# Optimization experiments

Measured on AMD Instinct MI355X. Metric: run time of the kernel, lower is better.

Reference implementation:

```python
import jax, jax.numpy as jnp
import numpy as np

N, E, F, B, L, C = 10000, 80000, 1024, 32, 800, 16
D = 128  # output_dim


def _lrelu(v):
    return jax.nn.leaky_relu(v, 0.01)


def _gcn(x, ei, W, b):
    # PyG GCNConv: add self-loops, symmetric norm D^-1/2 (A+I) D^-1/2, x@W then scatter, +bias
    loops = jnp.arange(N)
    row = jnp.concatenate([ei[0], loops])
    col = jnp.concatenate([ei[1], loops])
    deg = jax.ops.segment_sum(jnp.ones_like(row, x.dtype), col, num_segments=N)
    dinv = jnp.where(deg > 0, 1.0 / jnp.sqrt(jnp.maximum(deg, 1e-12)), 0.0)
    norm = dinv[row] * dinv[col]
    xw = x @ W  # [N,F]
    return jax.ops.segment_sum(xw[row] * norm[:, None], col, num_segments=N) + b


def _mean_pool(h, batch):
    s = jax.ops.segment_sum(h, batch, num_segments=B)
    c = jax.ops.segment_sum(jnp.ones((h.shape[0],), h.dtype), batch, num_segments=B)
    return s / jnp.maximum(c, 1.0)[:, None]


def _masif(ms, mf, sw, sb, fw, fb, Wfc, bfc):
    # mean over channels -> Conv1d(1,1,1) == scalar scale+shift -> relu
    s = jax.nn.relu(ms.mean(1) * sw[0] + sb[0])  # [B,L]
    f = jax.nn.relu(mf.mean(1) * fw[0] + fb[0])  # [B,L]
    m = jnp.stack([s, f], 1)                      # [B,2,L]
    m = m.reshape(B, 2, 80, L // 80).mean(-1)     # AdaptiveAvgPool1d(80), L % 80 == 0
    return m.mean(1) @ Wfc + bfc                  # [B,64]


def setup_inputs():
    key = jax.random.key(0)
    ks = jax.random.split(key, 48)
    def rn(i, shape, s=0.02):
        return jax.random.normal(ks[i], shape, jnp.float32) * s
    inp = {}
    inp['pro1_x'] = jax.random.normal(ks[0], (N, F), jnp.float32)
    inp['pro1_edge_index'] = jax.random.randint(ks[1], (2, E), 0, N)
    inp['pro1_batch'] = jnp.sort(jax.random.randint(ks[2], (N,), 0, B))
    inp['pro2_x'] = jax.random.normal(ks[3], (N, F), jnp.float32)
    inp['pro2_edge_index'] = jax.random.randint(ks[4], (2, E), 0, N)
    inp['pro2_batch'] = jnp.sort(jax.random.randint(ks[5], (N,), 0, B))
    for j, name in enumerate(['mas1_straight', 'mas1_flipped', 'mas2_straight', 'mas2_flipped']):
        inp[name] = jax.random.normal(ks[6 + j], (B, C, L), jnp.float32)
    inp['W_g1'] = rn(10, (F, F)); inp['b_g1'] = rn(11, (F,))
    inp['W_g2'] = rn(12, (F, F)); inp['b_g2'] = rn(13, (F,))
    inp['W_pf1'] = rn(14, (F, D)); inp['b_pf1'] = rn(15, (D,))
    inp['W_pf2'] = rn(16, (F, D)); inp['b_pf2'] = rn(17, (D,))
    inp['W_fc1'] = rn(18, (2 * D, 256)); inp['b_fc1'] = rn(19, (256,))
    inp['W_fc2'] = rn(20, (256, 64)); inp['b_fc2'] = rn(21, (64,))
    inp['cs1_w'] = rn(22, (1,), 1.0); inp['cs1_b'] = rn(23, (1,), 0.1)
    inp['cf1_w'] = rn(24, (1,), 1.0); inp['cf1_b'] = rn(25, (1,), 0.1)
    inp['cs2_w'] = rn(26, (1,), 1.0); inp['cs2_b'] = rn(27, (1,), 0.1)
    inp['cf2_w'] = rn(28, (1,), 1.0); inp['cf2_b'] = rn(29, (1,), 0.1)
    inp['W_m1'] = rn(30, (80, 64)); inp['b_m1'] = rn(31, (64,))
    inp['W_m2'] = rn(32, (80, 64)); inp['b_m2'] = rn(33, (64,))
    inp['W_out'] = rn(34, (192, 1)); inp['b_out'] = rn(35, (1,))
    return inp


def reference(pro1_x, pro1_edge_index, pro1_batch, pro2_x, pro2_edge_index, pro2_batch,
              mas1_straight, mas1_flipped, mas2_straight, mas2_flipped,
              W_g1, b_g1, W_g2, b_g2, W_pf1, b_pf1, W_pf2, b_pf2,
              W_fc1, b_fc1, W_fc2, b_fc2,
              cs1_w, cs1_b, cf1_w, cf1_b, cs2_w, cs2_b, cf2_w, cf2_b,
              W_m1, b_m1, W_m2, b_m2, W_out, b_out):
    # protein branch 1
    h1 = _lrelu(_gcn(pro1_x, pro1_edge_index, W_g1, b_g1))
    x1 = _lrelu(_mean_pool(h1, pro1_batch) @ W_pf1 + b_pf1)  # dropout = eval identity
    # protein branch 2
    h2 = _lrelu(_gcn(pro2_x, pro2_edge_index, W_g2, b_g2))
    x2 = _lrelu(_mean_pool(h2, pro2_batch) @ W_pf2 + b_pf2)
    xc = jnp.concatenate([x1, x2], 1)
    xc = _lrelu(xc @ W_fc1 + b_fc1)
    xc = _lrelu(xc @ W_fc2 + b_fc2)
    m1 = _masif(mas1_straight, mas1_flipped, cs1_w, cs1_b, cf1_w, cf1_b, W_m1, b_m1)
    m2 = _masif(mas2_straight, mas2_flipped, cs2_w, cs2_b, cf2_w, cf2_b, W_m2, b_m2)
    z = jnp.concatenate([xc, m1, m2], 1)  # [B,192]
    return jax.nn.sigmoid(z @ W_out + b_out)
```

## Files before the change

### kernel.cpp

```cpp
#include <hip/hip_runtime.h>
#include <hip/hip_bf16.h>
#include <math.h>

#define NNODES 10000
#define NEDGES 80000
#define FDIM   1024
#define BGR    32
#define LLEN   800
#define CCH    16
#define DDIM   128
#define NPAD2  10240
#define NE_BLK 625

typedef __attribute__((ext_vector_type(4))) _Float16 f16x4;
typedef __attribute__((ext_vector_type(8))) _Float16 f16x8;
typedef __attribute__((ext_vector_type(4))) float f32x4;
typedef __attribute__((ext_vector_type(2))) float f32x2;
typedef __attribute__((ext_vector_type(2))) long long2v;

__device__ __forceinline__ float lrelu(float v){ return v > 0.0f ? v : 0.01f*v; }

__global__ __launch_bounds__(256) void k_deg(const int* __restrict__ ei0, const int* __restrict__ ei1,
                                             int* __restrict__ cnt){
  int i = blockIdx.x*256 + threadIdx.x;
  int br = i >= NEDGES;
  int e  = br ? i - NEDGES : i;
  const int* ei = br ? ei1 : ei0;
  atomicAdd(&cnt[br*NNODES + ei[NEDGES + e]], 1);
}

__global__ __launch_bounds__(1024) void k_scan(const int* __restrict__ cnt, int* __restrict__ rowstart,
                                               float* __restrict__ dinv,
                                               const int* __restrict__ batch0,
                                               const int* __restrict__ batch1,
                                               int* __restrict__ bstart_){
  __shared__ int part[1024];
  const int br = blockIdx.x;
  const int* c = cnt + br*NNODES;
  int* rs = rowstart + br*(NNODES+1);
  float* dv = dinv + br*NNODES;
  const int* batch = br ? batch1 : batch0;
  int* bstart = bstart_ + br*(BGR+1);
  const int t = threadIdx.x;
  const int base = t*10;
  int local[10];
  int s = 0;
  #pragma unroll
  for (int i = 0; i < 10; ++i){
    int v = (base+i < NNODES) ? c[base+i] : 0;
    local[i] = s; s += v;
    if (base+i < NNODES) dv[base+i] = rsqrtf((float)v + 1.0f);
  }
  part[t] = s;
  __syncthreads();
  for (int off = 1; off < 1024; off <<= 1){
    int v = (t >= off) ? part[t-off] : 0;
    __syncthreads();
    part[t] += v;
    __syncthreads();
  }
  const int prev = (t == 0) ? 0 : part[t-1];
  #pragma unroll
  for (int i = 0; i < 10; ++i)
    if (base+i < NNODES) rs[base+i] = prev + local[i];
  if (t == 0) rs[NNODES] = NEDGES;
  for (int i = base; i < base+10 && i < NNODES; ++i){
    int b = batch[i];
    if (i == 0){ for (int bb = 0; bb <= b; ++bb) bstart[bb] = 0; }
    else {
      int pb = batch[i-1];
      if (b != pb) for (int bb = pb+1; bb <= b; ++bb) bstart[bb] = i;
    }
    if (i == NNODES-1){ for (int bb = b+1; bb <= BGR; ++bb) bstart[bb] = NNODES; }
  }
}

__global__ __launch_bounds__(256) void k_misc(const int* __restrict__ ei0, const int* __restrict__ ei1,
                                              const int* __restrict__ rowstart,
                                              int* __restrict__ cursor, int* __restrict__ csr,
                                              const float* __restrict__ x0, const float* __restrict__ x1,
                                              const float* __restrict__ dinv,
                                              unsigned char* __restrict__ xs8,
                                              const float* __restrict__ W0, const float* __restrict__ W1,
                                              unsigned char* __restrict__ Wt8,
                                              const float* __restrict__ ms1, const float* __restrict__ mf1,
                                              const float* __restrict__ ms2, const float* __restrict__ mf2,
                                              const float* __restrict__ sw1, const float* __restrict__ sb1,
                                              const float* __restrict__ fw1, const float* __restrict__ fb1,
                                              const float* __restrict__ sw2, const float* __restrict__ sb2,
                                              const float* __restrict__ fw2, const float* __restrict__ fb2,
                                              const float* __restrict__ Wm1, const float* __restrict__ bm1,
                                              const float* __restrict__ Wm2, const float* __restrict__ bm2,
                                              float* __restrict__ m12){
  __shared__ float tl[32][33];
  __shared__ float sf[LLEN];
  __shared__ float w80[80];
  const int bx = blockIdx.x, t = threadIdx.x;
  if (bx < NE_BLK){
    const int i = bx*256 + t;
    const int br = i >= NEDGES;
    const int e  = br ? i - NEDGES : i;
    const int* ei = br ? ei1 : ei0;
    const int r = ei[e], c = ei[NEDGES + e];
    const int pos = atomicAdd(&cursor[br*NNODES + c], 1);
    csr[br*NEDGES + rowstart[br*(NNODES+1) + c] + pos] = r;
  } else if (bx < NE_BLK + 2*NNODES){
    const int idx = bx - NE_BLK;
    const int br = idx >= NNODES;
    const int row = br ? idx - NNODES : idx;
    const float* x = (br ? x1 : x0) + (size_t)row*FDIM;
    unsigned char* o = xs8 + ((size_t)br*NNODES + row)*FDIM;
    const int f = t*4;
    const float d = dinv[br*NNODES + row];
    const float4 v = *(const float4*)(x + f);
    int p = __builtin_amdgcn_cvt_pk_fp8_f32(v.x*d, v.y*d, 0, false);
    p = __builtin_amdgcn_cvt_pk_fp8_f32(v.z*d, v.w*d, p, true);
    *(int*)(o + f) = p;
  } else if (bx < NE_BLK + 2*NNODES + 2048){
    const int idx = bx - NE_BLK - 2*NNODES;
    const int br = idx >> 10, tile = idx & 1023;
    const float* W = br ? W1 : W0;
    unsigned char* Wo = Wt8 + (size_t)br*FDIM*FDIM;
    const int k0 = (tile >> 5)*32, n0 = (tile & 31)*32;
    const int r = t >> 3, c4 = (t & 7)*4;
    const float4 v = *(const float4*)(W + (size_t)(k0+r)*FDIM + n0 + c4);
    tl[r][c4] = v.x; tl[r][c4+1] = v.y; tl[r][c4+2] = v.z; tl[r][c4+3] = v.w;
    __syncthreads();
    int p = __builtin_amdgcn_cvt_pk_fp8_f32(tl[c4  ][r], tl[c4+1][r], 0, false);
    p = __builtin_amdgcn_cvt_pk_fp8_f32(tl[c4+2][r], tl[c4+3][r], p, true);
    const int L = k0 + c4;
    const int g = L >> 6, u = (L >> 3) & 7, h = (L >> 2) & 1;
    const int Lp = g*64 + (2*(u&3) + (u>>2))*8 + h*4;
    *(int*)(Wo + (size_t)(n0+r)*FDIM + Lp) = p;
  } else {
    const int idx = bx - NE_BLK - 2*NNODES - 2048;
    const int br = idx >> 5, b = idx & 31;
    const float* ms = br ? ms2 : ms1;
    const float* mf = br ? mf2 : mf1;
    const float swv = (br ? sw2 : sw1)[0], sbv = (br ? sb2 : sb1)[0];
    const float fwv = (br ? fw2 : fw1)[0], fbv = (br ? fb2 : fb1)[0];
    const float* Wm = br ? Wm2 : Wm1;
    const float* bm = br ? bm2 : bm1;
    for (int l = t; l < LLEN; l += 256){
      float sm = 0.f, fm = 0.f;
      for (int c = 0; c < CCH; ++c){
        sm += ms[((size_t)b*CCH + c)*LLEN + l];
        fm += mf[((size_t)b*CCH + c)*LLEN + l];
      }
      sm = fmaxf(sm*(1.0f/16.0f)*swv + sbv, 0.f);
      fm = fmaxf(fm*(1.0f/16.0f)*fwv + fbv, 0.f);
      sf[l] = sm + fm;
    }
    __syncthreads();
    if (t < 80){
      float a = 0.f;
      for (int j = 0; j < 10; ++j) a += sf[t*10 + j];
      w80[t] = a * 0.05f;
    }
    __syncthreads();
    if (t < 64){
      float acc = bm[t];
      for (int k = 0; k < 80; ++k) acc += w80[k] * Wm[k*64 + t];
      m12[((size_t)br*BGR + b)*64 + t] = acc;
    }
  }
}

__global__ __launch_bounds__(256) void k_gath(const unsigned char* __restrict__ xs8_,
                                              const int* __restrict__ rowstart_,
                                              const int* __restrict__ csr_,
                                              const float* __restrict__ dinv_,
                                              unsigned char* __restrict__ xa8_){
  const int t = threadIdx.x;
  const int br = blockIdx.y;
  const int n = blockIdx.x*2 + (t >> 7);
  const int lt = t & 127;

  const unsigned char* xs8 = xs8_ + (size_t)br*NNODES*FDIM;
  const int* rowstart = rowstart_ + br*(NNODES+1);
  const int* csr = csr_ + br*NEDGES;
  const float* dinv = dinv_ + br*NNODES;
  unsigned char* xa8 = xa8_ + (size_t)br*NPAD2*FDIM;

  const int f = lt*8;
  const int g = lt >> 3, u = lt & 7;
  const int fp = g*64 + (2*(u&3) + (u>>2))*8;
  unsigned char* op = xa8 + (size_t)n*FDIM + fp;
  if (n >= NNODES){
    *(long*)op = 0L;
    return;
  }
  const int s0 = rowstart[n], s1 = rowstart[n+1];
  float a0=0,a1=0,a2=0,a3=0,a4=0,a5=0,a6=0,a7=0;
  auto addrow = [&](uint2 q){
    f32x2 w0 = __builtin_amdgcn_cvt_pk_f32_fp8((int)q.x, false);
    f32x2 w1 = __builtin_amdgcn_cvt_pk_f32_fp8((int)q.x, true);
    f32x2 w2 = __builtin_amdgcn_cvt_pk_f32_fp8((int)q.y, false);
    f32x2 w3 = __builtin_amdgcn_cvt_pk_f32_fp8((int)q.y, true);
    a0 += w0[0]; a1 += w0[1]; a2 += w1[0]; a3 += w1[1];
    a4 += w2[0]; a5 += w2[1]; a6 += w3[0]; a7 += w3[1];
  };
  addrow(*(const uint2*)(xs8 + (size_t)n*FDIM + f));
  int i = s0;
  for (; i + 4 <= s1; i += 4){
    const int r0 = csr[i], r1 = csr[i+1], r2 = csr[i+2], r3 = csr[i+3];
    const uint2 q0 = *(const uint2*)(xs8 + (size_t)r0*FDIM + f);
    const uint2 q1 = *(const uint2*)(xs8 + (size_t)r1*FDIM + f);
    const uint2 q2 = *(const uint2*)(xs8 + (size_t)r2*FDIM + f);
    const uint2 q3 = *(const uint2*)(xs8 + (size_t)r3*FDIM + f);
    addrow(q0); addrow(q1); addrow(q2); addrow(q3);
  }
  for (; i < s1; ++i){
    addrow(*(const uint2*)(xs8 + (size_t)csr[i]*FDIM + f));
  }
  const float d = dinv[n];
  uint2 o;
  int p0 = __builtin_amdgcn_cvt_pk_fp8_f32(a0*d, a1*d, 0, false);
  p0 = __builtin_amdgcn_cvt_pk_fp8_f32(a2*d, a3*d, p0, true);
  int p1 = __builtin_amdgcn_cvt_pk_fp8_f32(a4*d, a5*d, 0, false);
  p1 = __builtin_amdgcn_cvt_pk_fp8_f32(a6*d, a7*d, p1, true);
  o.x = (unsigned)p0; o.y = (unsigned)p1;
  *(uint2*)op = o;
}

__global__ __launch_bounds__(256) void k_gemm(const unsigned char* __restrict__ A_,
                                              const unsigned char* __restrict__ Bt_,
                                              const float* __restrict__ bg0,
                                              const float* __restrict__ bg1,
                                              const int* __restrict__ bstart_,
                                              float* __restrict__ pool_){
  __shared__ __align__(16) char smem[32768];
  const int id  = blockIdx.x;
  const int w   = (id & 7)*160 + (id >> 3);
  const int col = w & 7;
  const int ru  = w >> 3;
  const int row = ru % 80;
  const int br  = ru / 80;

  const unsigned char* A  = A_  + (size_t)br*NPAD2*FDIM;
  const unsigned char* Bt = Bt_ + (size_t)br*FDIM*FDIM;
  const float* bg = br ? bg1 : bg0;
  const int* bstart = bstart_ + br*(BGR+1);
  float* pool = pool_ + br*BGR*FDIM;

  const int row0 = row*128, col0 = col*128;
  const int tid  = threadIdx.x;
  const int lane = tid & 63, wave = tid >> 6;
  const int wm = wave >> 1, wn = wave & 1;
  const int lr = lane >> 2;
  const int ls = lane & 3;

  f32x4 acc[4][4] = {};

  auto stage = [&](int buf, int k0){
    char* Asb = smem + buf*8192;
    char* Bsb = smem + 16384 + buf*8192;
    #pragma unroll
    for (int j = 0; j < 2; ++j){
      const int r0 = wave*32 + j*16;
      const int ra = r0 + lr;
      const int sa = ls ^ ((ra >> 1) & 3);
      __builtin_amdgcn_global_load_lds(
        (const __attribute__((address_space(1))) void*)(A + (size_t)(row0+ra)*FDIM + k0 + sa*16),
        (__attribute__((address_space(3))) void*)(Asb + r0*64), 16, 0, 0);
      __builtin_amdgcn_global_load_lds(
        (const __attribute__((address_space(1))) void*)(Bt + (size_t)(col0+ra)*FDIM + k0 + sa*16),
        (__attribute__((address_space(3))) void*)(Bsb + r0*64), 16, 0, 0);
    }
  };

  auto compute = [&](int buf){
    const char* Asb = smem + buf*8192;
    const char* Bsb = smem + 16384 + buf*8192;
    long2v af[4], bf[4];
    const int s = lane >> 4;
    #pragma unroll
    for (int i = 0; i < 4; ++i){
      const int rA = wm*64 + i*16 + (lane & 15);
      af[i] = *(const long2v*)(Asb + rA*64 + ((s ^ ((rA>>1)&3))<<4));
      const int rB = wn*64 + i*16 + (lane & 15);
      bf[i] = *(const long2v*)(Bsb + rB*64 + ((s ^ ((rB>>1)&3))<<4));
    }
    #pragma unroll
    for (int mi = 0; mi < 4; ++mi)
      #pragma unroll
      for (int ni = 0; ni < 4; ++ni){
        acc[mi][ni] = __builtin_amdgcn_mfma_f32_16x16x32_fp8_fp8(af[mi][0], bf[ni][0], acc[mi][ni], 0, 0, 0);
        acc[mi][ni] = __builtin_amdgcn_mfma_f32_16x16x32_fp8_fp8(af[mi][1], bf[ni][1], acc[mi][ni], 0, 0, 0);
      }
  };

  stage(0, 0);
  #pragma unroll 2
  for (int ks = 0; ks < 16; ++ks){
    if (ks < 15){
      stage((ks+1)&1, (ks+1)*64);
      asm volatile("s_waitcnt vmcnt(4)" ::: "memory");
    } else {
      asm volatile("s_waitcnt vmcnt(0)" ::: "memory");
    }
    __builtin_amdgcn_s_barrier();
    compute(ks&1);
    __builtin_amdgcn_s_barrier();
  }
  __syncthreads();

  _Float16* sc = (_Float16*)smem;
  float bcol[4];
  #pragma unroll
  for (int ni = 0; ni < 4; ++ni) bcol[ni] = bg[col0 + wn*64 + ni*16 + (lane & 15)];
  #pragma unroll
  for (int mi = 0; mi < 4; ++mi){
    #pragma unroll
    for (int j = 0; j < 4; ++j){
      const int lrow = wm*64 + mi*16 + (lane>>4)*4 + j;
      const int valid = (row0 + lrow) < NNODES;
      #pragma unroll
      for (int ni = 0; ni < 4; ++ni){
        const int lcol = wn*64 + ni*16 + (lane & 15);
        sc[lrow*128 + lcol] = valid ? (_Float16)lrelu(acc[mi][ni][j] + bcol[ni]) : (_Float16)0.f;
      }
    }
  }
  __syncthreads();

  {
    const int c = tid & 127, h = tid >> 7;
    const int base = row0 + h*64;
    int rmax = NNODES - base; if (rmax > 64) rmax = 64;
    if (rmax > 0){
      int b = 0;
      while (bstart[b+1] <= base) ++b;
      int bs_next = bstart[b+1];
      float sum = 0.f;
      for (int r = 0; r < rmax; ++r){
        const int grow = base + r;
        while (grow >= bs_next){
          atomicAdd(&pool[b*FDIM + col0 + c], sum);
          sum = 0.f; ++b; bs_next = bstart[b+1];
        }
        sum += (float)sc[(h*64 + r)*128 + c];
      }
      atomicAdd(&pool[b*FDIM + col0 + c], sum);
    }
  }
}

__global__ __launch_bounds__(512) void k_pf(const float* __restrict__ pool_,
                                            const float* __restrict__ W0,
                                            const float* __restrict__ W1,
                                            const float* __restrict__ bias0,
                                            const float* __restrict__ bias1,
                                            const int* __restrict__ bstart_,
                                            float* __restrict__ x12){
  __shared__ float red[512];
  const int br = blockIdx.y, b = blockIdx.x, t = threadIdx.x;
  const int d = t & 127, kq = t >> 7;
  const float* W = (br ? W1 : W0) + (size_t)kq*256*DDIM + d;
  const float* pp = pool_ + (size_t)(br*BGR + b)*FDIM + kq*256;
  float acc = 0.f;
  #pragma unroll 4
  for (int kk = 0; kk < 256; kk += 4){
    const float4 pv = *(const float4*)(pp + kk);
    acc += pv.x * W[(kk  )*DDIM] + pv.y * W[(kk+1)*DDIM]
         + pv.z * W[(kk+2)*DDIM] + pv.w * W[(kk+3)*DDIM];
  }
  red[t] = acc;
  __syncthreads();
  if (t < 128){
    const int* bstart = bstart_ + br*(BGR+1);
    const int cntn = bstart[b+1] - bstart[b];
    const float inv = 1.0f / fmaxf((float)cntn, 1.0f);
    float a = (red[t] + red[t+128] + red[t+256] + red[t+384]) * inv + (br ? bias1 : bias0)[t];
    x12[((size_t)br*BGR + b)*DDIM + t] = lrelu(a);
  }
}

__global__ __launch_bounds__(256) void k_head(const float* __restrict__ x12,
                                              const float* __restrict__ Wfc1, const float* __restrict__ bfc1,
                                              const float* __restrict__ Wfc2, const float* __restrict__ bfc2,
                                              const float* __restrict__ m12,
                                              const float* __restrict__ Wout, const float* __restrict__ bout,
                                              float* __restrict__ out){
  __shared__ float xf[256];
  __shared__ float xc[64];
  __shared__ float red[192];
  const int b = blockIdx.x, t = threadIdx.x;
  const float* xin1 = x12 + (size_t)b*DDIM;
  const float* xin2 = x12 + (size_t)(BGR + b)*DDIM;
  float acc = bfc1[t];
  for (int k = 0; k < 128; ++k) acc += xin1[k] * Wfc1[k*256 + t];
  for (int k = 0; k < 128; ++k) acc += xin2[k] * Wfc1[(128+k)*256 + t];
  xf[t] = lrelu(acc);
  __syncthreads();
  if (t < 64){
    float a = bfc2[t];
    for (int k = 0; k < 256; ++k) a += xf[k] * Wfc2[k*64 + t];
    xc[t] = lrelu(a);
  }
  __syncthreads();
  if (t < 192){
    float v;
    if (t < 64)       v = xc[t] * Wout[t];
    else if (t < 128) v = m12[(size_t)b*64 + (t-64)] * Wout[t];
    else              v = m12[(size_t)(BGR + b)*64 + (t-128)] * Wout[t];
    red[t] = v;
  }
  __syncthreads();
  if (t == 0){
    float a = bout[0];
    for (int i = 0; i < 192; ++i) a += red[i];
    out[b] = 1.0f / (1.0f + expf(-a));
  }
}

extern "C" void kernel_launch(void* const* d_in, const int* in_sizes, int n_in,
                              void* d_out, int out_size, void* d_ws, size_t ws_size,
                              hipStream_t stream){
  const float* pro1_x = (const float*)d_in[0];
  const int*   ei1    = (const int*)d_in[1];
  const int*   batch1 = (const int*)d_in[2];
  const float* pro2_x = (const float*)d_in[3];
  const int*   ei2    = (const int*)d_in[4];
  const int*   batch2 = (const int*)d_in[5];
  const float* mas1_s = (const float*)d_in[6];
  const float* mas1_f = (const float*)d_in[7];
  const float* mas2_s = (const float*)d_in[8];
  const float* mas2_f = (const float*)d_in[9];
  const float* W_g1 = (const float*)d_in[10]; const float* b_g1 = (const float*)d_in[11];
  const float* W_g2 = (const float*)d_in[12]; const float* b_g2 = (const float*)d_in[13];
  const float* W_pf1= (const float*)d_in[14]; const float* b_pf1= (const float*)d_in[15];
  const float* W_pf2= (const float*)d_in[16]; const float* b_pf2= (const float*)d_in[17];
  const float* W_fc1= (const float*)d_in[18]; const float* b_fc1= (const float*)d_in[19];
  const float* W_fc2= (const float*)d_in[20]; const float* b_fc2= (const float*)d_in[21];
  const float* cs1w = (const float*)d_in[22]; const float* cs1b = (const float*)d_in[23];
  const float* cf1w = (const float*)d_in[24]; const float* cf1b = (const float*)d_in[25];
  const float* cs2w = (const float*)d_in[26]; const float* cs2b = (const float*)d_in[27];
  const float* cf2w = (const float*)d_in[28]; const float* cf2b = (const float*)d_in[29];
  const float* W_m1 = (const float*)d_in[30]; const float* b_m1 = (const float*)d_in[31];
  const float* W_m2 = (const float*)d_in[32]; const float* b_m2 = (const float*)d_in[33];
  const float* W_out= (const float*)d_in[34]; const float* b_out= (const float*)d_in[35];
  float* out = (float*)d_out;
  (void)in_sizes; (void)n_in; (void)out_size; (void)ws_size;

  char* p = (char*)d_ws;
  auto alloc = [&](size_t bytes)->char*{ char* r = p; p += (bytes + 255) & ~(size_t)255; return r; };
  int*   cntcur = (int*)alloc((size_t)4*NNODES*4);
  float* pool   = (float*)alloc((size_t)2*BGR*FDIM*4);
  int*   cnt    = cntcur;
  int*   cursor = cntcur + 2*NNODES;
  unsigned char* xs8 = (unsigned char*)alloc((size_t)2*NNODES*FDIM);
  unsigned char* xa8 = (unsigned char*)alloc((size_t)2*NPAD2*FDIM);
  unsigned char* Wt8 = (unsigned char*)alloc((size_t)2*FDIM*FDIM);
  float* dinv = (float*)alloc((size_t)2*NNODES*4);
  int*   rowstart = (int*)alloc((size_t)2*(NNODES+1)*4);
  int*   csr  = (int*)alloc((size_t)2*NEDGES*4);
  int*   bstart = (int*)alloc((size_t)2*(BGR+1)*4);
  float* x12  = (float*)alloc((size_t)2*BGR*DDIM*4);
  float* m12  = (float*)alloc((size_t)2*BGR*64*4);

  hipMemsetAsync(cntcur, 0, (size_t)4*NNODES*4 + (size_t)2*BGR*FDIM*4, stream);
  k_deg<<<NE_BLK, 256, 0, stream>>>(ei1, ei2, cnt);
  k_scan<<<2, 1024, 0, stream>>>(cnt, rowstart, dinv, batch1, batch2, bstart);
  k_misc<<<NE_BLK + 2*NNODES + 2048 + 64, 256, 0, stream>>>(
      ei1, ei2, rowstart, cursor, csr,
      pro1_x, pro2_x, dinv, xs8,
      W_g1, W_g2, Wt8,
      mas1_s, mas1_f, mas2_s, mas2_f,
      cs1w, cs1b, cf1w, cf1b,
      cs2w, cs2b, cf2w, cf2b,
      W_m1, b_m1, W_m2, b_m2, m12);
  k_gath<<<dim3(NPAD2/2, 2), 256, 0, stream>>>(xs8, rowstart, csr, dinv, xa8);
  k_gemm<<<1280, 256, 0, stream>>>(xa8, Wt8, b_g1, b_g2, bstart, pool);
  k_pf<<<dim3(BGR, 2), 512, 0, stream>>>(pool, W_pf1, W_pf2, b_pf1, b_pf2, bstart, x12);
  k_head<<<BGR, 256, 0, stream>>>(x12, W_fc1, b_fc1, W_fc2, b_fc2, m12, W_out, b_out, out);
}
```

Measured before the change: 156.5 us.

## Overlap branch-2 gather with branch-1 GEMM in a combined kernel

The gather and GEMM are split per branch. Branch 1 is gathered first. A combined kernel then runs branch-1 GEMM tiles and branch-2 gather blocks side by side, and a final kernel runs the branch-2 GEMM. The aim is to overlap the memory-bound gather with the compute-bound GEMM instead of running them back to back. It adds one kernel launch, and the mixed kernel's 32KB shared allocation may limit occupancy for the gather blocks.

Measured after the change: 171.9 us. 1.1x slower.

```diff
diff --git a/kernel.cpp b/kernel.cpp
--- a/kernel.cpp
+++ b/kernel.cpp
@@ -166,16 +166,11 @@
   }
 }
 
-__global__ __launch_bounds__(256) void k_gath(const unsigned char* __restrict__ xs8_,
-                                              const int* __restrict__ rowstart_,
-                                              const int* __restrict__ csr_,
-                                              const float* __restrict__ dinv_,
-                                              unsigned char* __restrict__ xa8_){
-  const int t = threadIdx.x;
-  const int br = blockIdx.y;
-  const int n = blockIdx.x*2 + (t >> 7);
-  const int lt = t & 127;
-
+__device__ __forceinline__ void gather_body(int n, int br, int lt,
+    const unsigned char* __restrict__ xs8_, const int* __restrict__ rowstart_,
+    const int* __restrict__ csr_, const float* __restrict__ dinv_,
+    unsigned char* __restrict__ xa8_)
+{
   const unsigned char* xs8 = xs8_ + (size_t)br*NNODES*FDIM;
   const int* rowstart = rowstart_ + br*(NNODES+1);
   const int* csr = csr_ + br*NEDGES;
@@ -223,19 +218,14 @@
   *(uint2*)op = o;
 }
 
-__global__ __launch_bounds__(256) void k_gemm(const unsigned char* __restrict__ A_,
-                                              const unsigned char* __restrict__ Bt_,
-                                              const float* __restrict__ bg0,
-                                              const float* __restrict__ bg1,
-                                              const int* __restrict__ bstart_,
-                                              float* __restrict__ pool_){
-  __shared__ __align__(16) char smem[32768];
-  const int id  = blockIdx.x;
-  const int w   = (id & 7)*160 + (id >> 3);
+__device__ __forceinline__ void gemm_pool_tile(int id, int br, char* smem,
+    const unsigned char* __restrict__ A_, const unsigned char* __restrict__ Bt_,
+    const float* __restrict__ bg0, const float* __restrict__ bg1,
+    const int* __restrict__ bstart_, float* __restrict__ pool_)
+{
+  const int w   = (id & 7)*80 + (id >> 3);
   const int col = w & 7;
-  const int ru  = w >> 3;
-  const int row = ru % 80;
-  const int br  = ru / 80;
+  const int row = w >> 3;
 
   const unsigned char* A  = A_  + (size_t)br*NPAD2*FDIM;
   const unsigned char* Bt = Bt_ + (size_t)br*FDIM*FDIM;
@@ -344,6 +334,46 @@
       atomicAdd(&pool[b*FDIM + col0 + c], sum);
     }
   }
+}
+
+__global__ __launch_bounds__(256) void k_gath0(const unsigned char* __restrict__ xs8,
+                                               const int* __restrict__ rowstart,
+                                               const int* __restrict__ csr,
+                                               const float* __restrict__ dinv,
+                                               unsigned char* __restrict__ xa8){
+  const int t = threadIdx.x;
+  const int n = blockIdx.x*2 + (t >> 7);
+  gather_body(n, 0, t & 127, xs8, rowstart, csr, dinv, xa8);
+}
+
+__global__ __launch_bounds__(256) void k_gg(const unsigned char* __restrict__ xa8,
+                                            const unsigned char* __restrict__ Wt8,
+                                            const float* __restrict__ bg0,
+                                            const float* __restrict__ bg1,
+                                            const int* __restrict__ bstart,
+                                            float* __restrict__ pool,
+                                            const unsigned char* __restrict__ xs8,
+                                            const int* __restrict__ rowstart,
+                                            const int* __restrict__ csr,
+                                            const float* __restrict__ dinv){
+  __shared__ __align__(16) char smem[32768];
+  const int bx = blockIdx.x, t = threadIdx.x;
+  if (bx < 640){
+    gemm_pool_tile(bx, 0, smem, xa8, Wt8, bg0, bg1, bstart, pool);
+  } else {
+    const int n = (bx - 640)*2 + (t >> 7);
+    gather_body(n, 1, t & 127, xs8, rowstart, csr, dinv, (unsigned char*)xa8);
+  }
+}
+
+__global__ __launch_bounds__(256) void k_gemm1(const unsigned char* __restrict__ xa8,
+                                               const unsigned char* __restrict__ Wt8,
+                                               const float* __restrict__ bg0,
+                                               const float* __restrict__ bg1,
+                                               const int* __restrict__ bstart,
+                                               float* __restrict__ pool){
+  __shared__ __align__(16) char smem[32768];
+  gemm_pool_tile(blockIdx.x, 1, smem, xa8, Wt8, bg0, bg1, bstart, pool);
 }
 
 __global__ __launch_bounds__(512) void k_pf(const float* __restrict__ pool_,
@@ -470,8 +500,10 @@
       cs1w, cs1b, cf1w, cf1b,
       cs2w, cs2b, cf2w, cf2b,
       W_m1, b_m1, W_m2, b_m2, m12);
-  k_gath<<<dim3(NPAD2/2, 2), 256, 0, stream>>>(xs8, rowstart, csr, dinv, xa8);
-  k_gemm<<<1280, 256, 0, stream>>>(xa8, Wt8, b_g1, b_g2, bstart, pool);
+  k_gath0<<<NPAD2/2, 256, 0, stream>>>(xs8, rowstart, csr, dinv, xa8);
+  k_gg<<<640 + NPAD2/2, 256, 0, stream>>>(xa8, Wt8, b_g1, b_g2, bstart, pool,
+                                          xs8, rowstart, csr, dinv);
+  k_gemm1<<<640, 256, 0, stream>>>(xa8, Wt8, b_g1, b_g2, bstart, pool);
   k_pf<<<dim3(BGR, 2), 512, 0, stream>>>(pool, W_pf1, W_pf2, b_pf1, b_pf2, bstart, x12);
   k_head<<<BGR, 256, 0, stream>>>(x12, W_fc1, b_fc1, W_fc2, b_fc2, m12, W_out, b_out, out);
 }
```

## Split masif channel reduction across more blocks and reorder block dispatch in k_misc

Applied to the files above, without the earlier changes.

The masif branch was 64 long-running blocks placed at the tail of k_misc, each summing 16 channels over 800 positions. They are now 256 blocks that each reduce a quarter of the channels into partial buffers. These blocks are dispatched first so they do not straggle at the end of the grid. The partial sums are combined, and the relu, pooling and small matmul applied, in k_head. This adds extra global traffic for the partials and serial work in the 32-block head kernel.

Result: no change. 155.5 us (-0.6%).

```diff
diff --git a/kernel.cpp b/kernel.cpp
--- a/kernel.cpp
+++ b/kernel.cpp
@@ -11,6 +11,7 @@
 #define DDIM   128
 #define NPAD2  10240
 #define NE_BLK 625
+#define MAS_BLK 256
 
 typedef __attribute__((ext_vector_type(4))) _Float16 f16x4;
 typedef __attribute__((ext_vector_type(8))) _Float16 f16x8;
@@ -85,39 +86,36 @@
                                               unsigned char* __restrict__ Wt8,
                                               const float* __restrict__ ms1, const float* __restrict__ mf1,
                                               const float* __restrict__ ms2, const float* __restrict__ mf2,
-                                              const float* __restrict__ sw1, const float* __restrict__ sb1,
-                                              const float* __restrict__ fw1, const float* __restrict__ fb1,
-                                              const float* __restrict__ sw2, const float* __restrict__ sb2,
-                                              const float* __restrict__ fw2, const float* __restrict__ fb2,
-                                              const float* __restrict__ Wm1, const float* __restrict__ bm1,
-                                              const float* __restrict__ Wm2, const float* __restrict__ bm2,
-                                              float* __restrict__ m12){
+                                              float* __restrict__ spart, float* __restrict__ fpart){
   __shared__ float tl[32][33];
-  __shared__ float sf[LLEN];
-  __shared__ float w80[80];
   const int bx = blockIdx.x, t = threadIdx.x;
-  if (bx < NE_BLK){
-    const int i = bx*256 + t;
+  if (bx < MAS_BLK){
+    const int idx = bx;
+    const int br = idx >> 7, rem = idx & 127;
+    const int b = rem >> 2, q = rem & 3;
+    const float* ms = br ? ms2 : ms1;
+    const float* mf = br ? mf2 : mf1;
+    float* sp = spart + (((size_t)br*BGR + b)*4 + q)*LLEN;
+    float* fp = fpart + (((size_t)br*BGR + b)*4 + q)*LLEN;
+    for (int l = t; l < LLEN; l += 256){
+      float sm = 0.f, fm = 0.f;
+      #pragma unroll
+      for (int c = 0; c < 4; ++c){
+        sm += ms[((size_t)b*CCH + q*4 + c)*LLEN + l];
+        fm += mf[((size_t)b*CCH + q*4 + c)*LLEN + l];
+      }
+      sp[l] = sm; fp[l] = fm;
+    }
+  } else if (bx < MAS_BLK + NE_BLK){
+    const int i = (bx - MAS_BLK)*256 + t;
     const int br = i >= NEDGES;
     const int e  = br ? i - NEDGES : i;
     const int* ei = br ? ei1 : ei0;
     const int r = ei[e], c = ei[NEDGES + e];
     const int pos = atomicAdd(&cursor[br*NNODES + c], 1);
     csr[br*NEDGES + rowstart[br*(NNODES+1) + c] + pos] = r;
-  } else if (bx < NE_BLK + 2*NNODES){
-    const int idx = bx - NE_BLK;
-    const int br = idx >= NNODES;
-    const int row = br ? idx - NNODES : idx;
-    const float* x = (br ? x1 : x0) + (size_t)row*FDIM;
-    unsigned char* o = xs8 + ((size_t)br*NNODES + row)*FDIM;
-    const int f = t*4;
-    const float d = dinv[br*NNODES + row];
-    const float4 v = *(const float4*)(x + f);
-    int p = __builtin_amdgcn_cvt_pk_fp8_f32(v.x*d, v.y*d, 0, false);
-    p = __builtin_amdgcn_cvt_pk_fp8_f32(v.z*d, v.w*d, p, true);
-    *(int*)(o + f) = p;
-  } else if (bx < NE_BLK + 2*NNODES + 2048){
-    const int idx = bx - NE_BLK - 2*NNODES;
+  } else if (bx < MAS_BLK + NE_BLK + 2048){
+    const int idx = bx - MAS_BLK - NE_BLK;
     const int br = idx >> 10, tile = idx & 1023;
     const float* W = br ? W1 : W0;
     unsigned char* Wo = Wt8 + (size_t)br*FDIM*FDIM;
@@ -133,36 +131,17 @@
     const int Lp = g*64 + (2*(u&3) + (u>>2))*8 + h*4;
     *(int*)(Wo + (size_t)(n0+r)*FDIM + Lp) = p;
   } else {
-    const int idx = bx - NE_BLK - 2*NNODES - 2048;
-    const int br = idx >> 5, b = idx & 31;
-    const float* ms = br ? ms2 : ms1;
-    const float* mf = br ? mf2 : mf1;
-    const float swv = (br ? sw2 : sw1)[0], sbv = (br ? sb2 : sb1)[0];
-    const float fwv = (br ? fw2 : fw1)[0], fbv = (br ? fb2 : fb1)[0];
-    const float* Wm = br ? Wm2 : Wm1;
-    const float* bm = br ? bm2 : bm1;
-    for (int l = t; l < LLEN; l += 256){
-      float sm = 0.f, fm = 0.f;
-      for (int c = 0; c < CCH; ++c){
-        sm += ms[((size_t)b*CCH + c)*LLEN + l];
-        fm += mf[((size_t)b*CCH + c)*LLEN + l];
-      }
-      sm = fmaxf(sm*(1.0f/16.0f)*swv + sbv, 0.f);
-      fm = fmaxf(fm*(1.0f/16.0f)*fwv + fbv, 0.f);
-      sf[l] = sm + fm;
-    }
-    __syncthreads();
-    if (t < 80){
-      float a = 0.f;
-      for (int j = 0; j < 10; ++j) a += sf[t*10 + j];
-      w80[t] = a * 0.05f;
-    }
-    __syncthreads();
-    if (t < 64){
-      float acc = bm[t];
-      for (int k = 0; k < 80; ++k) acc += w80[k] * Wm[k*64 + t];
-      m12[((size_t)br*BGR + b)*64 + t] = acc;
-    }
+    const int idx = bx - MAS_BLK - NE_BLK - 2048;
+    const int br = idx >= NNODES;
+    const int row = br ? idx - NNODES : idx;
+    const float* x = (br ? x1 : x0) + (size_t)row*FDIM;
+    unsigned char* o = xs8 + ((size_t)br*NNODES + row)*FDIM;
+    const int f = t*4;
+    const float d = dinv[br*NNODES + row];
+    const float4 v = *(const float4*)(x + f);
+    int p = __builtin_amdgcn_cvt_pk_fp8_f32(v.x*d, v.y*d, 0, false);
+    p = __builtin_amdgcn_cvt_pk_fp8_f32(v.z*d, v.w*d, p, true);
+    *(int*)(o + f) = p;
   }
 }
 
@@ -379,13 +358,53 @@
 __global__ __launch_bounds__(256) void k_head(const float* __restrict__ x12,
                                               const float* __restrict__ Wfc1, const float* __restrict__ bfc1,
                                               const float* __restrict__ Wfc2, const float* __restrict__ bfc2,
-                                              const float* __restrict__ m12,
+                                              const float* __restrict__ spart, const float* __restrict__ fpart,
+                                              const float* __restrict__ sw1, const float* __restrict__ sb1,
+                                              const float* __restrict__ fw1, const float* __restrict__ fb1,
+                                              const float* __restrict__ sw2, const float* __restrict__ sb2,
+                                              const float* __restrict__ fw2, const float* __restrict__ fb2,
+                                              const float* __restrict__ Wm1, const float* __restrict__ bm1,
+                                              const float* __restrict__ Wm2, const float* __restrict__ bm2,
                                               const float* __restrict__ Wout, const float* __restrict__ bout,
                                               float* __restrict__ out){
+  __shared__ float sf[LLEN];
+  __shared__ float w80[80];
+  __shared__ float mm[2][64];
   __shared__ float xf[256];
   __shared__ float xc[64];
   __shared__ float red[192];
   const int b = blockIdx.x, t = threadIdx.x;
+
+  #pragma unroll
+  for (int br = 0; br < 2; ++br){
+    const float swv = (br ? sw2 : sw1)[0], sbv = (br ? sb2 : sb1)[0];
+    const float fwv = (br ? fw2 : fw1)[0], fbv = (br ? fb2 : fb1)[0];
+    const float* Wm = br ? Wm2 : Wm1;
+    const float* bm = br ? bm2 : bm1;
+    const float* sp = spart + ((size_t)br*BGR + b)*4*LLEN;
+    const float* fp = fpart + ((size_t)br*BGR + b)*4*LLEN;
+    for (int l = t; l < LLEN; l += 256){
+      float sm = sp[l] + sp[LLEN + l] + sp[2*LLEN + l] + sp[3*LLEN + l];
+      float fm = fp[l] + fp[LLEN + l] + fp[2*LLEN + l] + fp[3*LLEN + l];
+      sm = fmaxf(sm*(1.0f/16.0f)*swv + sbv, 0.f);
+      fm = fmaxf(fm*(1.0f/16.0f)*fwv + fbv, 0.f);
+      sf[l] = sm + fm;
+    }
+    __syncthreads();
+    if (t < 80){
+      float a = 0.f;
+      for (int j = 0; j < 10; ++j) a += sf[t*10 + j];
+      w80[t] = a * 0.05f;
+    }
+    __syncthreads();
+    if (t < 64){
+      float a = bm[t];
+      for (int k = 0; k < 80; ++k) a += w80[k] * Wm[k*64 + t];
+      mm[br][t] = a;
+    }
+    __syncthreads();
+  }
+
   const float* xin1 = x12 + (size_t)b*DDIM;
   const float* xin2 = x12 + (size_t)(BGR + b)*DDIM;
   float acc = bfc1[t];
@@ -402,8 +421,8 @@
   if (t < 192){
     float v;
     if (t < 64)       v = xc[t] * Wout[t];
-    else if (t < 128) v = m12[(size_t)b*64 + (t-64)] * Wout[t];
-    else              v = m12[(size_t)(BGR + b)*64 + (t-128)] * Wout[t];
+    else if (t < 128) v = mm[0][t-64] * Wout[t];
+    else              v = mm[1][t-128] * Wout[t];
     red[t] = v;
   }
   __syncthreads();
@@ -457,21 +476,25 @@
   int*   csr  = (int*)alloc((size_t)2*NEDGES*4);
   int*   bstart = (int*)alloc((size_t)2*(BGR+1)*4);
   float* x12  = (float*)alloc((size_t)2*BGR*DDIM*4);
-  float* m12  = (float*)alloc((size_t)2*BGR*64*4);
+  float* spart = (float*)alloc((size_t)2*BGR*4*LLEN*4);
+  float* fpart = (float*)alloc((size_t)2*BGR*4*LLEN*4);
 
   hipMemsetAsync(cntcur, 0, (size_t)4*NNODES*4 + (size_t)2*BGR*FDIM*4, stream);
   k_deg<<<NE_BLK, 256, 0, stream>>>(ei1, ei2, cnt);
   k_scan<<<2, 1024, 0, stream>>>(cnt, rowstart, dinv, batch1, batch2, bstart);
-  k_misc<<<NE_BLK + 2*NNODES + 2048 + 64, 256, 0, stream>>>(
+  k_misc<<<MAS_BLK + NE_BLK + 2048 + 2*NNODES, 256, 0, stream>>>(
       ei1, ei2, rowstart, cursor, csr,
       pro1_x, pro2_x, dinv, xs8,
       W_g1, W_g2, Wt8,
       mas1_s, mas1_f, mas2_s, mas2_f,
-      cs1w, cs1b, cf1w, cf1b,
-      cs2w, cs2b, cf2w, cf2b,
-      W_m1, b_m1, W_m2, b_m2, m12);
+      spart, fpart);
   k_gath<<<dim3(NPAD2/2, 2), 256, 0, stream>>>(xs8, rowstart, csr, dinv, xa8);
   k_gemm<<<1280, 256, 0, stream>>>(xa8, Wt8, b_g1, b_g2, bstart, pool);
   k_pf<<<dim3(BGR, 2), 512, 0, stream>>>(pool, W_pf1, W_pf2, b_pf1, b_pf2, bstart, x12);
-  k_head<<<BGR, 256, 0, stream>>>(x12, W_fc1, b_fc1, W_fc2, b_fc2, m12, W_out, b_out, out);
-}
+  k_head<<<BGR, 256, 0, stream>>>(x12, W_fc1, b_fc1, W_fc2, b_fc2,
+                                  spart, fpart,
+                                  cs1w, cs1b, cf1w, cf1b,
+                                  cs2w, cs2b, cf2w, cf2b,
+                                  W_m1, b_m1, W_m2, b_m2,
+                                  W_out, b_out, out);
+}
```
